# Kernel optimization log

Measured on AMD Instinct MI355X. Metric: run time of the kernel, lower is better.

## Reference

```python
import jax, jax.numpy as jnp
import numpy as np


def _conv(x, w, b, pad):
    y = jax.lax.conv_general_dilated(x, w, window_strides=(1, 1),
                                     padding=[(pad, pad), (pad, pad)],
                                     dimension_numbers=('NCHW', 'OIHW', 'NCHW'))
    return y + b[None, :, None, None]


def _kernel_normalizer(mask, k):
    # softmax over the k*k kernel taps; hamming=1 so the renorm is a numerical no-op (kept faithful)
    n, mck2, h, w = mask.shape
    mc = mck2 // (k * k)
    m = jax.nn.softmax(mask.reshape(n, mc, k * k, h, w), axis=2)
    m = m / jnp.sum(m, axis=2, keepdims=True)
    return m.reshape(n, mck2, h, w)


def _carafe(feat, mask, k, g, s):
    # CARAFE: out[n,c,i,j] = sum_{ki,kj} mask[n, grp*k*k + ki*k + kj, i, j] * feat[n, c, i//s+ki-r, j//s+kj-r]
    n, c, h, w = feat.shape
    r = (k - 1) // 2
    cg = c // g
    hs, ws = h * s, w * s
    pad = jnp.pad(feat, ((0, 0), (0, 0), (r, r), (r, r)))
    m = mask.reshape(n, g, k * k, hs, ws)
    out = jnp.zeros((n, g, cg, hs, ws), feat.dtype)
    idx = 0
    for ki in range(k):
        for kj in range(k):
            sh = pad[:, :, ki:ki + h, kj:kj + w]
            if s > 1:
                sh = jnp.repeat(jnp.repeat(sh, s, axis=2), s, axis=3)
            out = out + sh.reshape(n, g, cg, hs, ws) * m[:, :, idx][:, :, None]
            idx += 1
    return out.reshape(n, c, hs, ws)


def setup_inputs() -> dict:
    key = jax.random.key(0)
    ks = jax.random.split(key, 8)
    N, CH, CL, H, W, CC = 4, 256, 256, 128, 128, 64
    KL, KH, EK = 5, 3, 3

    def w_init(k, shape):
        fan_in = shape[1] * shape[2] * shape[3]
        return jax.random.normal(k, shape, jnp.float32) * (1.0 / np.sqrt(fan_in))

    return {
        'hr_feat': jax.random.normal(ks[0], (N, CH, H, W), jnp.float32),
        'lr_feat': jax.random.normal(ks[1], (N, CL, H // 2, W // 2), jnp.float32),
        'hr_w': w_init(ks[2], (CC, CH, 1, 1)), 'hr_b': jnp.zeros((CC,), jnp.float32),
        'lr_w': w_init(ks[3], (CC, CL, 1, 1)), 'lr_b': jnp.zeros((CC,), jnp.float32),
        'enc_w': w_init(ks[4], (KL * KL, CC, EK, EK)), 'enc_b': jnp.zeros((KL * KL,), jnp.float32),
        'enc2_w': w_init(ks[5], (KH * KH, CC, EK, EK)), 'enc2_b': jnp.zeros((KH * KH,), jnp.float32),
    }


def reference(hr_feat, lr_feat, hr_w, hr_b, lr_w, lr_b, enc_w, enc_b, enc2_w, enc2_b):
    KL, KH, G = 5, 3, 1
    chf = _conv(hr_feat, hr_w, hr_b, 0)
    clf = _conv(lr_feat, lr_w, lr_b, 0)
    mask_hr_hr = _conv(chf, enc2_w, enc2_b, 1)
    mask_hr_init = _kernel_normalizer(mask_hr_hr, KH)
    chf = chf + chf - _carafe(chf, mask_hr_init, KH, G, 1)
    mask_lr_hr = _conv(chf, enc_w, enc_b, 1)
    mask_lr_init = _kernel_normalizer(mask_lr_hr, KL)
    mask_lr_lr_lr = _conv(clf, enc_w, enc_b, 1)
    # carafe scale-2 output is already hr-sized -> F.interpolate(nearest, hr size) is identity
    mask_lr_lr = _carafe(mask_lr_lr_lr, mask_lr_init, KL, G, 2)
    mask_lr = mask_lr_hr + mask_lr_lr
    mask_lr_init = _kernel_normalizer(mask_lr, KL)
    mask_hr_lr = _carafe(_conv(clf, enc2_w, enc2_b, 1), mask_lr_init, KL, G, 2)
    mask_hr = mask_hr_hr + mask_hr_lr
    mask_lr_out = _kernel_normalizer(mask_lr, KL)
    lr_out = _carafe(lr_feat, mask_lr_out, KL, G, 2)
    mask_hr_out = _kernel_normalizer(mask_hr, KH)
    hr_out = (hr_feat - _carafe(hr_feat, mask_hr_out, KH, G, 1)) + hr_feat
    return (mask_lr_out, hr_out, lr_out)
```

## Files before the change

### kernel.cpp

```cpp
#include <hip/hip_runtime.h>
#include <hip/hip_bf16.h>

typedef __hip_bfloat16 bf16;

constexpr int Nn  = 4;
constexpr int Ci  = 256;
constexpr int Cc  = 64;
constexpr int Hh  = 128;
constexpr int Ww  = 128;
constexpr int HWh = Hh * Ww;
constexpr int Hl  = 64;
constexpr int Wl  = 64;
constexpr int HWl = Hl * Wl;
constexpr int K2L = 25;
constexpr int K2H = 9;

constexpr size_t OFF_MASK = 0;
constexpr size_t OFF_HR   = (size_t)Nn * K2L * HWh;
constexpr size_t OFF_LR   = OFF_HR + (size_t)Nn * Ci * HWh;

constexpr size_t A_CHF    = 0;
constexpr size_t A_MLRHR  = 0;
constexpr size_t A_MLRLL  = 1700000;
constexpr size_t A_CLFE2  = 2200000;
constexpr size_t A_MHRRAW = 4100000;
constexpr size_t A_WHR    = 7800000;
constexpr size_t A_WLR    = 7820000;
constexpr size_t A_WENC   = 7840000;
constexpr size_t A_WENC2  = 7860000;
constexpr size_t A_BHR    = 7870000;
constexpr size_t A_BLR    = 7870100;
constexpr size_t A_BENC   = 7870200;
constexpr size_t A_BENC2  = 7870300;

constexpr size_t B_CLF    = 0;
constexpr size_t B_CHF2   = 1100000;
constexpr size_t B_MHRHR  = 5300000;
constexpr size_t B_MLR    = 0;

__device__ __forceinline__ float tofloat(float v) { return v; }
__device__ __forceinline__ float tofloat(bf16 v) { return __bfloat162float(v); }

template<typename T> __device__ __forceinline__ T fromfloat(float v);
template<> __device__ __forceinline__ float fromfloat<float>(float v) { return v; }
template<> __device__ __forceinline__ bf16  fromfloat<bf16>(float v)  { return __float2bfloat16(v); }

__device__ __forceinline__ float* scrp(void* d, int f32, size_t reg, size_t off) {
  float* b = f32 ? ((float*)d + reg) : (float*)((bf16*)d + reg);
  return b + off;
}

__global__ void detect_dtype(const void* feat, int* flag) {
  __shared__ int s;
  if (threadIdx.x == 0) s = 0;
  __syncthreads();
  unsigned short b = ((const unsigned short*)feat)[threadIdx.x];
  float v = __uint_as_float(((unsigned int)b) << 16);
  if (!(fabsf(v) < 1000.0f)) atomicOr(&s, 1);
  __syncthreads();
  if (threadIdx.x == 0) *flag = s;
}

template<typename T>
__device__ void prep_body(const T* hw, const T* hb, const T* lw, const T* lb,
                          const T* ew, const T* eb, const T* e2w, const T* e2b,
                          float* whr, float* wlr, float* wenc, float* wenc2,
                          float* bhr, float* blr, float* benc, float* benc2) {
  int tid = blockIdx.x * 256 + threadIdx.x, nt = gridDim.x * 256;
  for (int i = tid; i < Cc * Ci; i += nt) {
    int co = i / Ci, ci = i % Ci;
    whr[ci * Cc + co] = tofloat(hw[i]);
    wlr[ci * Cc + co] = tofloat(lw[i]);
  }
  for (int i = tid; i < K2L * Cc * 9; i += nt) {
    int ko = i / (Cc * 9), r = i % (Cc * 9), ci = r / 9, k = r % 9;
    wenc[(ci * K2L + ko) * 9 + k] = tofloat(ew[i]);
  }
  for (int i = tid; i < K2H * Cc * 9; i += nt) {
    int ko = i / (Cc * 9), r = i % (Cc * 9), ci = r / 9, k = r % 9;
    wenc2[(ci * K2H + ko) * 9 + k] = tofloat(e2w[i]);
  }
  if (tid < Cc)  { bhr[tid] = tofloat(hb[tid]); blr[tid] = tofloat(lb[tid]); }
  if (tid < K2L) benc[tid]  = tofloat(eb[tid]);
  if (tid < K2H) benc2[tid] = tofloat(e2b[tid]);
}

__global__ void prep_weights(const int* flag, void* dout,
                             const void* hw, const void* hb, const void* lw, const void* lb,
                             const void* ew, const void* eb, const void* e2w, const void* e2b) {
  int f32 = *flag;
  float* whr   = scrp(dout, f32, OFF_LR, A_WHR);
  float* wlr   = scrp(dout, f32, OFF_LR, A_WLR);
  float* wenc  = scrp(dout, f32, OFF_LR, A_WENC);
  float* wenc2 = scrp(dout, f32, OFF_LR, A_WENC2);
  float* bhr   = scrp(dout, f32, OFF_LR, A_BHR);
  float* blr   = scrp(dout, f32, OFF_LR, A_BLR);
  float* benc  = scrp(dout, f32, OFF_LR, A_BENC);
  float* benc2 = scrp(dout, f32, OFF_LR, A_BENC2);
  if (f32) prep_body<float>((const float*)hw, (const float*)hb, (const float*)lw, (const float*)lb,
                            (const float*)ew, (const float*)eb, (const float*)e2w, (const float*)e2b,
                            whr, wlr, wenc, wenc2, bhr, blr, benc, benc2);
  else     prep_body<bf16>((const bf16*)hw, (const bf16*)hb, (const bf16*)lw, (const bf16*)lb,
                           (const bf16*)ew, (const bf16*)eb, (const bf16*)e2w, (const bf16*)e2b,
                           whr, wlr, wenc, wenc2, bhr, blr, benc, benc2);
}

template<typename T, int CW>
__device__ void conv1x1_body(const T* __restrict__ in, const float* __restrict__ wt,
                             const float* __restrict__ bias, float* __restrict__ out, int P) {
  const int tid = threadIdx.x;
  const int n = blockIdx.z;
  const int pbase = blockIdx.x * 64 + (tid & 63);
  const int co0 = __builtin_amdgcn_readfirstlane(blockIdx.y * 4 * CW + ((tid >> 6) * CW));
  const T* inp = in + (size_t)n * Ci * P + pbase;

  float acc[CW];
  #pragma unroll
  for (int c = 0; c < CW; ++c) acc[c] = bias[co0 + c];

  #pragma unroll 4
  for (int ci = 0; ci < Ci; ++ci) {
    float v = tofloat(inp[(size_t)ci * P]);
    const float* wr = wt + ci * Cc + co0;
    #pragma unroll
    for (int c = 0; c < CW; ++c) acc[c] = fmaf(v, wr[c], acc[c]);
  }
  float* op = out + (size_t)n * Cc * P + pbase;
  #pragma unroll
  for (int c = 0; c < CW; ++c) op[(size_t)(co0 + c) * P] = acc[c];
}

template<int CW>
__global__ __launch_bounds__(256) void conv1x1_k(const int* flag, void* dout, const void* in,
                                                 size_t w_off, size_t b_off,
                                                 size_t o_reg, size_t o_off, int P) {
  int f32 = __builtin_amdgcn_readfirstlane(*flag);
  const float* wt   = scrp(dout, f32, OFF_LR, w_off);
  const float* bias = scrp(dout, f32, OFF_LR, b_off);
  float* out        = scrp(dout, f32, o_reg, o_off);
  if (f32) conv1x1_body<float, CW>((const float*)in, wt, bias, out, P);
  else     conv1x1_body<bf16, CW>((const bf16*)in, wt, bias, out, P);
}

template<int KO, int KOG>
__device__ __forceinline__ void conv3x3_body(const float* __restrict__ in,
                                             const float* __restrict__ wt,
                                             const float* __restrict__ bias,
                                             float* __restrict__ out,
                                             int hh, int ww, int n, int ko0, float* tile) {
  const int tid = threadIdx.x;
  const int tx = tid & 15, ty = tid >> 4;
  const int bx = blockIdx.x * 16, by = blockIdx.y * 16;

  float acc[KOG];
  #pragma unroll
  for (int ko = 0; ko < KOG; ++ko) acc[ko] = bias[ko0 + ko];

  for (int cc = 0; cc < Cc; cc += 16) {
    __syncthreads();
    for (int i = tid; i < 16 * 18 * 18; i += 256) {
      int ci = i / 324, r = i % 324, yy = r / 18, xx = r % 18;
      int gy = by + yy - 1, gx = bx + xx - 1;
      float v = 0.f;
      if (gy >= 0 && gy < hh && gx >= 0 && gx < ww)
        v = in[(((size_t)n * Cc + cc + ci) * hh + gy) * ww + gx];
      tile[i] = v;
    }
    __syncthreads();
    for (int ci = 0; ci < 16; ++ci) {
      float nb[9];
      #pragma unroll
      for (int dy = 0; dy < 3; ++dy)
        #pragma unroll
        for (int dx = 0; dx < 3; ++dx)
          nb[dy * 3 + dx] = tile[ci * 324 + (ty + dy) * 18 + tx + dx];
      const float* wr = wt + ((size_t)(cc + ci) * KO + ko0) * 9;
      #pragma unroll
      for (int ko = 0; ko < KOG; ++ko)
        #pragma unroll
        for (int k = 0; k < 9; ++k)
          acc[ko] = fmaf(wr[ko * 9 + k], nb[k], acc[ko]);
    }
  }
  const size_t ob = (((size_t)n * KO + ko0) * hh + by + ty) * ww + bx + tx;
  #pragma unroll
  for (int ko = 0; ko < KOG; ++ko) out[ob + (size_t)ko * hh * ww] = acc[ko];
}

template<int KO, int KOG>
__global__ __launch_bounds__(256) void conv3x3_k(const int* flag, void* dout,
                                                 size_t i_reg, size_t i_off,
                                                 size_t w_off, size_t b_off,
                                                 size_t o_reg, size_t o_off, int hh, int ww) {
  const int f32 = __builtin_amdgcn_readfirstlane(*flag);
  const float* in   = scrp(dout, f32, i_reg, i_off);
  const float* wt   = scrp(dout, f32, OFF_LR, w_off);
  const float* bias = scrp(dout, f32, OFF_LR, b_off);
  float* out        = scrp(dout, f32, o_reg, o_off);

  constexpr int NG = KO / KOG;
  __shared__ float tile[16 * 18 * 18];
  const int n = blockIdx.z / NG;
  const int ko0 = (blockIdx.z % NG) * KOG;
  conv3x3_body<KO, KOG>(in, wt, bias, out, hh, ww, n, ko0, tile);
}

__global__ __launch_bounds__(256) void conv3x3_dual_k(const int* flag, void* dout) {
  const int f32 = __builtin_amdgcn_readfirstlane(*flag);
  const float* in    = scrp(dout, f32, OFF_HR, B_CLF);
  const float* wenc  = scrp(dout, f32, OFF_LR, A_WENC);
  const float* benc  = scrp(dout, f32, OFF_LR, A_BENC);
  const float* wenc2 = scrp(dout, f32, OFF_LR, A_WENC2);
  const float* benc2 = scrp(dout, f32, OFF_LR, A_BENC2);
  float* out_ll  = scrp(dout, f32, OFF_LR, A_MLRLL);
  float* out_e2  = scrp(dout, f32, OFF_LR, A_CLFE2);

  __shared__ float tile[16 * 18 * 18];
  const int g = blockIdx.z % 8;
  const int n = blockIdx.z / 8;
  if (g < 5) conv3x3_body<K2L, 5>(in, wenc, benc, out_ll, Hl, Wl, n, g * 5, tile);
  else       conv3x3_body<K2H, 3>(in, wenc2, benc2, out_e2, Hl, Wl, n, (g - 5) * 3, tile);
}

template<int K2>
__global__ __launch_bounds__(256) void softmax_k(const int* flag, void* dout,
                                                 size_t i_reg, size_t i_off) {
  int f32 = __builtin_amdgcn_readfirstlane(*flag);
  const float* in = scrp(dout, f32, i_reg, i_off);
  const int p = blockIdx.x * blockDim.x + threadIdx.x;
  const int n = blockIdx.y;
  const float* ip = in + (size_t)n * K2 * HWh + p;
  float v[K2], m = -1e30f;
  #pragma unroll
  for (int k = 0; k < K2; ++k) { v[k] = ip[(size_t)k * HWh]; m = fmaxf(m, v[k]); }
  float s = 0.f;
  #pragma unroll
  for (int k = 0; k < K2; ++k) { v[k] = __expf(v[k] - m); s += v[k]; }
  const float inv = 1.0f / s;
  #pragma unroll
  for (int k = 0; k < K2; ++k) v[k] *= inv;

  const size_t g = (size_t)n * K2 * HWh + p;
  if (f32) {
    float* o = (float*)dout;
    #pragma unroll
    for (int k = 0; k < K2; ++k) o[g + (size_t)k * HWh] = v[k];
  } else {
    bf16* o = (bf16*)dout;
    #pragma unroll
    for (int k = 0; k < K2; ++k) o[g + (size_t)k * HWh] = fromfloat<bf16>(v[k]);
  }
}

template<typename FT, typename OT, int FINAL, int SM>
__device__ void carafe1_body(const FT* __restrict__ feat, const float* __restrict__ mask,
                             void* dout, size_t out_reg, float* outscr, int C, int CPB) {
  const int tid = threadIdx.x;
  const int tx = tid & 15, ty = tid >> 4;
  const int bx = blockIdx.x * 16, by = blockIdx.y * 16;
  const int numCG = C / CPB;
  const int n = blockIdx.z / numCG, cg = blockIdx.z % numCG;
  const int x = bx + tx, y = by + ty;

  float mv[9];
  #pragma unroll
  for (int k = 0; k < 9; ++k)
    mv[k] = mask[(((size_t)n * 9 + k) * Hh + y) * Ww + x];
  if (SM) {
    float m = -1e30f;
    #pragma unroll
    for (int k = 0; k < 9; ++k) m = fmaxf(m, mv[k]);
    float s = 0.f;
    #pragma unroll
    for (int k = 0; k < 9; ++k) { mv[k] = __expf(mv[k] - m); s += mv[k]; }
    const float inv = 1.0f / s;
    #pragma unroll
    for (int k = 0; k < 9; ++k) mv[k] *= inv;
  }

  const int c0 = cg * CPB;
  for (int c = c0; c < c0 + CPB; ++c) {
    const FT* fp = feat + ((size_t)n * C + c) * HWh;
    float s = 0.f, center = 0.f;
    #pragma unroll
    for (int dy = -1; dy <= 1; ++dy)
      #pragma unroll
      for (int dx = -1; dx <= 1; ++dx) {
        int yy = y + dy, xx = x + dx;
        float fv = 0.f;
        if (yy >= 0 && yy < Hh && xx >= 0 && xx < Ww) fv = tofloat(fp[yy * Ww + xx]);
        if (dy == 0 && dx == 0) center = fv;
        s = fmaf(fv, mv[(dy + 1) * 3 + (dx + 1)], s);
      }
    float r = 2.f * center - s;
    const size_t li = ((size_t)n * C + c) * HWh + y * Ww + x;
    if (FINAL) ((OT*)dout)[out_reg + li] = fromfloat<OT>(r);
    else       outscr[li] = r;
  }
}

__global__ __launch_bounds__(256) void carafe1_scr_k(const int* flag, void* dout,
    size_t f_reg, size_t f_off, size_t m_reg, size_t m_off, size_t o_reg, size_t o_off,
    int C, int CPB) {
  int f32 = __builtin_amdgcn_readfirstlane(*flag);
  carafe1_body<float, float, 0, 1>(scrp(dout, f32, f_reg, f_off), scrp(dout, f32, m_reg, m_off),
                                   dout, 0, scrp(dout, f32, o_reg, o_off), C, CPB);
}

__global__ __launch_bounds__(256) void carafe1_io_k(const int* flag, void* dout, const void* feat,
    size_t m_reg, size_t m_off, size_t out_reg, int C, int CPB) {
  int f32 = __builtin_amdgcn_readfirstlane(*flag);
  const float* m = scrp(dout, f32, m_reg, m_off);
  if (f32) carafe1_body<float, float, 1, 1>((const float*)feat, m, dout, out_reg, nullptr, C, CPB);
  else     carafe1_body<bf16, bf16, 1, 1>((const bf16*)feat, m, dout, out_reg, nullptr, C, CPB);
}

template<typename FT, typename MT, typename OT, int ADD, int FINAL, int SM>
__device__ void carafe2_body(const FT* __restrict__ feat, const MT* __restrict__ mask,
                             const float* __restrict__ addend, void* dout, size_t out_reg,
                             float* outscr, int C, int CPB) {
  __shared__ float ft[8][144];
  const int tid = threadIdx.x;
  const int tx = tid & 15, ty = tid >> 4;
  const int bx = blockIdx.x * 16, by = blockIdx.y * 16;
  const int numCG = C / CPB;
  const int n = blockIdx.z / numCG, cg = blockIdx.z % numCG;
  const int x = bx + tx, y = by + ty;

  float mv[25];
  #pragma unroll
  for (int k = 0; k < 25; ++k)
    mv[k] = tofloat(mask[(((size_t)n * 25 + k) * Hh + y) * Ww + x]);
  if (SM) {
    float m = -1e30f;
    #pragma unroll
    for (int k = 0; k < 25; ++k) m = fmaxf(m, mv[k]);
    float s = 0.f;
    #pragma unroll
    for (int k = 0; k < 25; ++k) { mv[k] = __expf(mv[k] - m); s += mv[k]; }
    const float inv = 1.0f / s;
    #pragma unroll
    for (int k = 0; k < 25; ++k) mv[k] *= inv;
  }

  const int fy0 = (by >> 1) - 2, fx0 = (bx >> 1) - 2;
  const int fyb = (ty >> 1) + 2, fxb = (tx >> 1) + 2;
  const int c0 = cg * CPB;

  for (int cb = 0; cb < CPB; cb += 8) {
    const int lim = (CPB - cb < 8) ? (CPB - cb) : 8;
    __syncthreads();
    for (int i = tid; i < lim * 144; i += 256) {
      int cc = i / 144, r = i % 144, fy = r / 12, fx = r % 12;
      int gy = fy0 + fy, gx = fx0 + fx;
      float v = 0.f;
      if (gy >= 0 && gy < Hl && gx >= 0 && gx < Wl)
        v = tofloat(feat[((size_t)n * C + c0 + cb + cc) * HWl + gy * Wl + gx]);
      ft[cc][r] = v;
    }
    __syncthreads();
    for (int cc = 0; cc < lim; ++cc) {
      float s = 0.f;
      #pragma unroll
      for (int ki = 0; ki < 5; ++ki)
        #pragma unroll
        for (int kj = 0; kj < 5; ++kj)
          s = fmaf(ft[cc][(fyb + ki - 2) * 12 + (fxb + kj - 2)], mv[ki * 5 + kj], s);
      const size_t li = (((size_t)n * C + c0 + cb + cc) * Hh + y) * Ww + x;
      float r = ADD ? (addend[li] + s) : s;
      if (FINAL) ((OT*)dout)[out_reg + li] = fromfloat<OT>(r);
      else       outscr[li] = r;
    }
  }
}

__global__ __launch_bounds__(256) void carafe2_scr_k(const int* flag, void* dout,
    size_t f_reg, size_t f_off, size_t m_reg, size_t m_off, size_t a_reg, size_t a_off,
    size_t o_reg, size_t o_off, int C, int CPB) {
  int f32 = __builtin_amdgcn_readfirstlane(*flag);
  carafe2_body<float, float, float, 1, 0, 1>(scrp(dout, f32, f_reg, f_off), scrp(dout, f32, m_reg, m_off),
      scrp(dout, f32, a_reg, a_off), dout, 0, scrp(dout, f32, o_reg, o_off), C, CPB);
}

__global__ __launch_bounds__(256) void carafe2_m0_k(const int* flag, void* dout,
    size_t f_reg, size_t f_off, size_t a_reg, size_t a_off, size_t o_reg, size_t o_off,
    int C, int CPB) {
  int f32 = __builtin_amdgcn_readfirstlane(*flag);
  const float* f = scrp(dout, f32, f_reg, f_off);
  const float* a = scrp(dout, f32, a_reg, a_off);
  float* o = scrp(dout, f32, o_reg, o_off);
  if (f32) carafe2_body<float, float, float, 1, 0, 0>(f, (const float*)dout, a, dout, 0, o, C, CPB);
  else     carafe2_body<float, bf16, float, 1, 0, 0>(f, (const bf16*)dout, a, dout, 0, o, C, CPB);
}

__global__ __launch_bounds__(256) void carafe2_io_k(const int* flag, void* dout, const void* feat,
    size_t out_reg, int C, int CPB) {
  int f32 = __builtin_amdgcn_readfirstlane(*flag);
  if (f32) carafe2_body<float, float, float, 0, 1, 0>((const float*)feat, (const float*)dout,
      nullptr, dout, out_reg, nullptr, C, CPB);
  else     carafe2_body<bf16, bf16, bf16, 0, 1, 0>((const bf16*)feat, (const bf16*)dout,
      nullptr, dout, out_reg, nullptr, C, CPB);
}

extern "C" void kernel_launch(void* const* d_in, const int* in_sizes, int n_in,
                              void* d_out, int out_size, void* d_ws, size_t ws_size,
                              hipStream_t stream) {
  const void* hr_feat = d_in[0];
  const void* lr_feat = d_in[1];
  int* flag = (int*)d_ws;

  detect_dtype<<<1, 256, 0, stream>>>(hr_feat, flag);
  prep_weights<<<64, 256, 0, stream>>>(flag, d_out, d_in[2], d_in[3], d_in[4], d_in[5],
                                       d_in[6], d_in[7], d_in[8], d_in[9]);
  conv1x1_k<16><<<dim3(HWh / 64, 1, Nn), 256, 0, stream>>>(flag, d_out, hr_feat, A_WHR, A_BHR, OFF_LR, A_CHF, HWh);
  conv1x1_k<8><<<dim3(HWl / 64, 2, Nn), 256, 0, stream>>>(flag, d_out, lr_feat, A_WLR, A_BLR, OFF_HR, B_CLF, HWl);
  conv3x3_k<K2H, 3><<<dim3(8, 8, Nn * 3), 256, 0, stream>>>(flag, d_out, OFF_LR, A_CHF, A_WENC2, A_BENC2, OFF_HR, B_MHRHR, Hh, Ww);
  carafe1_scr_k<<<dim3(8, 8, Nn * (Cc / 16)), 256, 0, stream>>>(flag, d_out, OFF_LR, A_CHF, OFF_HR, B_MHRHR, OFF_HR, B_CHF2, Cc, 16);
  conv3x3_k<K2L, 5><<<dim3(8, 8, Nn * 5), 256, 0, stream>>>(flag, d_out, OFF_HR, B_CHF2, A_WENC, A_BENC, OFF_LR, A_MLRHR, Hh, Ww);
  conv3x3_dual_k<<<dim3(4, 4, Nn * 8), 256, 0, stream>>>(flag, d_out);
  carafe2_scr_k<<<dim3(8, 8, Nn * 5), 256, 0, stream>>>(flag, d_out, OFF_LR, A_MLRLL, OFF_LR, A_MLRHR,
                                                        OFF_LR, A_MLRHR, OFF_HR, B_MLR, K2L, 5);
  softmax_k<K2L><<<dim3(HWh / 128, Nn), 128, 0, stream>>>(flag, d_out, OFF_HR, B_MLR);
  carafe2_m0_k<<<dim3(8, 8, Nn * 3), 256, 0, stream>>>(flag, d_out, OFF_LR, A_CLFE2,
                                                       OFF_HR, B_MHRHR, OFF_LR, A_MHRRAW, K2H, 3);
  carafe1_io_k<<<dim3(8, 8, Nn * (Ci / 32)), 256, 0, stream>>>(flag, d_out, hr_feat,
                                                               OFF_LR, A_MHRRAW, OFF_HR, Ci, 32);
  carafe2_io_k<<<dim3(8, 8, Nn * (Ci / 32)), 256, 0, stream>>>(flag, d_out, lr_feat, OFF_LR, Ci, 32);
}
```

Before: 575.7 us.

## Fuse conv launches, fold softmax into carafe2, add interior fast paths

Merges the two 1x1 convolutions into one launch and merges the hr 3x3 encoder conv with the dual lr 3x3 conv into one launch using flattened block indices. The standalone softmax kernel is removed: carafe2_m0 now reads the raw mask_lr, normalises it in-kernel and writes the final mask_lr_out from its first channel group. Interior tiles skip the bounds checks in the conv3x3, carafe1 and carafe2 loads. Scratch offsets are moved so the fused kernels do not overwrite each other's buffers. This cuts launch count and one full pass over the mask, at the cost of more code paths and a redundant softmax per channel group.

```diff
diff --git a/kernel.cpp b/kernel.cpp
--- a/kernel.cpp
+++ b/kernel.cpp
@@ -21,9 +21,9 @@
 
 constexpr size_t A_CHF    = 0;
 constexpr size_t A_MLRHR  = 0;
-constexpr size_t A_MLRLL  = 1700000;
-constexpr size_t A_CLFE2  = 2200000;
-constexpr size_t A_MHRRAW = 4100000;
+constexpr size_t A_MLRLL  = 4300000;
+constexpr size_t A_CLFE2  = 4800000;
+constexpr size_t A_MHRRAW = 5000000;
 constexpr size_t A_WHR    = 7800000;
 constexpr size_t A_WLR    = 7820000;
 constexpr size_t A_WENC   = 7840000;
@@ -106,14 +106,10 @@
 }
 
 template<typename T, int CW>
-__device__ void conv1x1_body(const T* __restrict__ in, const float* __restrict__ wt,
-                             const float* __restrict__ bias, float* __restrict__ out, int P) {
-  const int tid = threadIdx.x;
-  const int n = blockIdx.z;
-  const int pbase = blockIdx.x * 64 + (tid & 63);
-  const int co0 = __builtin_amdgcn_readfirstlane(blockIdx.y * 4 * CW + ((tid >> 6) * CW));
+__device__ __forceinline__ void conv1x1_core(const T* __restrict__ in, const float* __restrict__ wt,
+                                             const float* __restrict__ bias, float* __restrict__ out,
+                                             int P, int n, int pbase, int co0) {
   const T* inp = in + (size_t)n * Ci * P + pbase;
-
   float acc[CW];
   #pragma unroll
   for (int c = 0; c < CW; ++c) acc[c] = bias[co0 + c];
@@ -130,16 +126,31 @@
   for (int c = 0; c < CW; ++c) op[(size_t)(co0 + c) * P] = acc[c];
 }
 
-template<int CW>
-__global__ __launch_bounds__(256) void conv1x1_k(const int* flag, void* dout, const void* in,
-                                                 size_t w_off, size_t b_off,
-                                                 size_t o_reg, size_t o_off, int P) {
-  int f32 = __builtin_amdgcn_readfirstlane(*flag);
-  const float* wt   = scrp(dout, f32, OFF_LR, w_off);
-  const float* bias = scrp(dout, f32, OFF_LR, b_off);
-  float* out        = scrp(dout, f32, o_reg, o_off);
-  if (f32) conv1x1_body<float, CW>((const float*)in, wt, bias, out, P);
-  else     conv1x1_body<bf16, CW>((const bf16*)in, wt, bias, out, P);
+__global__ __launch_bounds__(256) void conv1x1_both_k(const int* flag, void* dout,
+                                                      const void* hr, const void* lr) {
+  const int f32 = __builtin_amdgcn_readfirstlane(*flag);
+  const float* whr = scrp(dout, f32, OFF_LR, A_WHR);
+  const float* wlr = scrp(dout, f32, OFF_LR, A_WLR);
+  const float* bhr = scrp(dout, f32, OFF_LR, A_BHR);
+  const float* blr = scrp(dout, f32, OFF_LR, A_BLR);
+  float* ochf = scrp(dout, f32, OFF_LR, A_CHF);
+  float* oclf = scrp(dout, f32, OFF_HR, B_CLF);
+  const int tid = threadIdx.x;
+  int b = blockIdx.x;
+  if (b < Nn * 256) {
+    const int n = b >> 8, xb = b & 255;
+    const int pbase = xb * 64 + (tid & 63);
+    const int co0 = __builtin_amdgcn_readfirstlane((tid >> 6) * 16);
+    if (f32) conv1x1_core<float, 16>((const float*)hr, whr, bhr, ochf, HWh, n, pbase, co0);
+    else     conv1x1_core<bf16, 16>((const bf16*)hr, whr, bhr, ochf, HWh, n, pbase, co0);
+  } else {
+    b -= Nn * 256;
+    const int n = b >> 7, rem = b & 127;
+    const int pbase = (rem & 63) * 64 + (tid & 63);
+    const int co0 = __builtin_amdgcn_readfirstlane((rem >> 6) * 32 + (tid >> 6) * 8);
+    if (f32) conv1x1_core<float, 8>((const float*)lr, wlr, blr, oclf, HWl, n, pbase, co0);
+    else     conv1x1_core<bf16, 8>((const bf16*)lr, wlr, blr, oclf, HWl, n, pbase, co0);
+  }
 }
 
 template<int KO, int KOG>
@@ -147,10 +158,11 @@
                                              const float* __restrict__ wt,
                                              const float* __restrict__ bias,
                                              float* __restrict__ out,
-                                             int hh, int ww, int n, int ko0, float* tile) {
+                                             int hh, int ww, int n, int ko0,
+                                             int bx, int by, float* tile) {
   const int tid = threadIdx.x;
   const int tx = tid & 15, ty = tid >> 4;
-  const int bx = blockIdx.x * 16, by = blockIdx.y * 16;
+  const bool inter = (bx >= 16) && (by >= 16) && (bx + 32 <= ww) && (by + 32 <= hh);
 
   float acc[KOG];
   #pragma unroll
@@ -158,13 +170,20 @@
 
   for (int cc = 0; cc < Cc; cc += 16) {
     __syncthreads();
-    for (int i = tid; i < 16 * 18 * 18; i += 256) {
-      int ci = i / 324, r = i % 324, yy = r / 18, xx = r % 18;
-      int gy = by + yy - 1, gx = bx + xx - 1;
-      float v = 0.f;
-      if (gy >= 0 && gy < hh && gx >= 0 && gx < ww)
-        v = in[(((size_t)n * Cc + cc + ci) * hh + gy) * ww + gx];
-      tile[i] = v;
+    if (inter) {
+      for (int i = tid; i < 16 * 324; i += 256) {
+        int ci = i / 324, r = i % 324, yy = r / 18, xx = r % 18;
+        tile[i] = in[(((size_t)n * Cc + cc + ci) * hh + by + yy - 1) * ww + bx + xx - 1];
+      }
+    } else {
+      for (int i = tid; i < 16 * 324; i += 256) {
+        int ci = i / 324, r = i % 324, yy = r / 18, xx = r % 18;
+        int gy = by + yy - 1, gx = bx + xx - 1;
+        float v = 0.f;
+        if (gy >= 0 && gy < hh && gx >= 0 && gx < ww)
+          v = in[(((size_t)n * Cc + cc + ci) * hh + gy) * ww + gx];
+        tile[i] = v;
+      }
     }
     __syncthreads();
     for (int ci = 0; ci < 16; ++ci) {
@@ -199,56 +218,36 @@
   float* out        = scrp(dout, f32, o_reg, o_off);
 
   constexpr int NG = KO / KOG;
-  __shared__ float tile[16 * 18 * 18];
+  __shared__ float tile[16 * 324];
   const int n = blockIdx.z / NG;
   const int ko0 = (blockIdx.z % NG) * KOG;
-  conv3x3_body<KO, KOG>(in, wt, bias, out, hh, ww, n, ko0, tile);
-}
-
-__global__ __launch_bounds__(256) void conv3x3_dual_k(const int* flag, void* dout) {
+  conv3x3_body<KO, KOG>(in, wt, bias, out, hh, ww, n, ko0, blockIdx.x * 16, blockIdx.y * 16, tile);
+}
+
+__global__ __launch_bounds__(256) void fused_s3_k(const int* flag, void* dout) {
   const int f32 = __builtin_amdgcn_readfirstlane(*flag);
-  const float* in    = scrp(dout, f32, OFF_HR, B_CLF);
+  const float* chf   = scrp(dout, f32, OFF_LR, A_CHF);
+  const float* clf   = scrp(dout, f32, OFF_HR, B_CLF);
   const float* wenc  = scrp(dout, f32, OFF_LR, A_WENC);
   const float* benc  = scrp(dout, f32, OFF_LR, A_BENC);
   const float* wenc2 = scrp(dout, f32, OFF_LR, A_WENC2);
   const float* benc2 = scrp(dout, f32, OFF_LR, A_BENC2);
-  float* out_ll  = scrp(dout, f32, OFF_LR, A_MLRLL);
-  float* out_e2  = scrp(dout, f32, OFF_LR, A_CLFE2);
-
-  __shared__ float tile[16 * 18 * 18];
-  const int g = blockIdx.z % 8;
-  const int n = blockIdx.z / 8;
-  if (g < 5) conv3x3_body<K2L, 5>(in, wenc, benc, out_ll, Hl, Wl, n, g * 5, tile);
-  else       conv3x3_body<K2H, 3>(in, wenc2, benc2, out_e2, Hl, Wl, n, (g - 5) * 3, tile);
-}
-
-template<int K2>
-__global__ __launch_bounds__(256) void softmax_k(const int* flag, void* dout,
-                                                 size_t i_reg, size_t i_off) {
-  int f32 = __builtin_amdgcn_readfirstlane(*flag);
-  const float* in = scrp(dout, f32, i_reg, i_off);
-  const int p = blockIdx.x * blockDim.x + threadIdx.x;
-  const int n = blockIdx.y;
-  const float* ip = in + (size_t)n * K2 * HWh + p;
-  float v[K2], m = -1e30f;
-  #pragma unroll
-  for (int k = 0; k < K2; ++k) { v[k] = ip[(size_t)k * HWh]; m = fmaxf(m, v[k]); }
-  float s = 0.f;
-  #pragma unroll
-  for (int k = 0; k < K2; ++k) { v[k] = __expf(v[k] - m); s += v[k]; }
-  const float inv = 1.0f / s;
-  #pragma unroll
-  for (int k = 0; k < K2; ++k) v[k] *= inv;
-
-  const size_t g = (size_t)n * K2 * HWh + p;
-  if (f32) {
-    float* o = (float*)dout;
-    #pragma unroll
-    for (int k = 0; k < K2; ++k) o[g + (size_t)k * HWh] = v[k];
+  float* o_mhrhr = scrp(dout, f32, OFF_HR, B_MHRHR);
+  float* o_ll    = scrp(dout, f32, OFF_LR, A_MLRLL);
+  float* o_e2    = scrp(dout, f32, OFF_LR, A_CLFE2);
+  __shared__ float tile[16 * 324];
+  int b = blockIdx.x;
+  if (b < Nn * 3 * 64) {
+    const int z = b >> 6, rem = b & 63;
+    conv3x3_body<K2H, 3>(chf, wenc2, benc2, o_mhrhr, Hh, Ww, z / 3, (z % 3) * 3,
+                         (rem & 7) * 16, (rem >> 3) * 16, tile);
   } else {
-    bf16* o = (bf16*)dout;
-    #pragma unroll
-    for (int k = 0; k < K2; ++k) o[g + (size_t)k * HWh] = fromfloat<bf16>(v[k]);
+    b -= Nn * 3 * 64;
+    const int z = b >> 4, rem = b & 15;
+    const int bx = (rem & 3) * 16, by = (rem >> 2) * 16;
+    const int g = z & 7, n = z >> 3;
+    if (g < 5) conv3x3_body<K2L, 5>(clf, wenc, benc, o_ll, Hl, Wl, n, g * 5, bx, by, tile);
+    else       conv3x3_body<K2H, 3>(clf, wenc2, benc2, o_e2, Hl, Wl, n, (g - 5) * 3, bx, by, tile);
   }
 }
 
@@ -261,6 +260,7 @@
   const int numCG = C / CPB;
   const int n = blockIdx.z / numCG, cg = blockIdx.z % numCG;
   const int x = bx + tx, y = by + ty;
+  const bool inter = (bx >= 16) && (by >= 16) && (bx + 32 <= Ww) && (by + 32 <= Hh);
 
   float mv[9];
   #pragma unroll
@@ -279,23 +279,40 @@
   }
 
   const int c0 = cg * CPB;
-  for (int c = c0; c < c0 + CPB; ++c) {
-    const FT* fp = feat + ((size_t)n * C + c) * HWh;
-    float s = 0.f, center = 0.f;
-    #pragma unroll
-    for (int dy = -1; dy <= 1; ++dy)
+  if (inter) {
+    for (int c = c0; c < c0 + CPB; ++c) {
+      const FT* fp = feat + ((size_t)n * C + c) * HWh + (size_t)y * Ww + x;
+      float center = tofloat(fp[0]);
+      float s = 0.f;
       #pragma unroll
-      for (int dx = -1; dx <= 1; ++dx) {
-        int yy = y + dy, xx = x + dx;
-        float fv = 0.f;
-        if (yy >= 0 && yy < Hh && xx >= 0 && xx < Ww) fv = tofloat(fp[yy * Ww + xx]);
-        if (dy == 0 && dx == 0) center = fv;
-        s = fmaf(fv, mv[(dy + 1) * 3 + (dx + 1)], s);
-      }
-    float r = 2.f * center - s;
-    const size_t li = ((size_t)n * C + c) * HWh + y * Ww + x;
-    if (FINAL) ((OT*)dout)[out_reg + li] = fromfloat<OT>(r);
-    else       outscr[li] = r;
+      for (int dy = -1; dy <= 1; ++dy)
+        #pragma unroll
+        for (int dx = -1; dx <= 1; ++dx)
+          s = fmaf(tofloat(fp[dy * Ww + dx]), mv[(dy + 1) * 3 + (dx + 1)], s);
+      float r = 2.f * center - s;
+      const size_t li = ((size_t)n * C + c) * HWh + (size_t)y * Ww + x;
+      if (FINAL) ((OT*)dout)[out_reg + li] = fromfloat<OT>(r);
+      else       outscr[li] = r;
+    }
+  } else {
+    for (int c = c0; c < c0 + CPB; ++c) {
+      const FT* fp = feat + ((size_t)n * C + c) * HWh;
+      float s = 0.f, center = 0.f;
+      #pragma unroll
+      for (int dy = -1; dy <= 1; ++dy)
+        #pragma unroll
+        for (int dx = -1; dx <= 1; ++dx) {
+          int yy = y + dy, xx = x + dx;
+          float fv = 0.f;
+          if (yy >= 0 && yy < Hh && xx >= 0 && xx < Ww) fv = tofloat(fp[yy * Ww + xx]);
+          if (dy == 0 && dx == 0) center = fv;
+          s = fmaf(fv, mv[(dy + 1) * 3 + (dx + 1)], s);
+        }
+      float r = 2.f * center - s;
+      const size_t li = ((size_t)n * C + c) * HWh + (size_t)y * Ww + x;
+      if (FINAL) ((OT*)dout)[out_reg + li] = fromfloat<OT>(r);
+      else       outscr[li] = r;
+    }
   }
 }
 
@@ -315,7 +332,7 @@
   else     carafe1_body<bf16, bf16, 1, 1>((const bf16*)feat, m, dout, out_reg, nullptr, C, CPB);
 }
 
-template<typename FT, typename MT, typename OT, int ADD, int FINAL, int SM>
+template<typename FT, typename MT, typename OT, typename MOT, int ADD, int FINAL, int SM, int WMASK>
 __device__ void carafe2_body(const FT* __restrict__ feat, const MT* __restrict__ mask,
                              const float* __restrict__ addend, void* dout, size_t out_reg,
                              float* outscr, int C, int CPB) {
@@ -326,6 +343,7 @@
   const int numCG = C / CPB;
   const int n = blockIdx.z / numCG, cg = blockIdx.z % numCG;
   const int x = bx + tx, y = by + ty;
+  const bool inter = (bx >= 16) && (by >= 16) && (bx + 32 <= Ww) && (by + 32 <= Hh);
 
   float mv[25];
   #pragma unroll
@@ -342,6 +360,12 @@
     #pragma unroll
     for (int k = 0; k < 25; ++k) mv[k] *= inv;
   }
+  if (WMASK && cg == 0) {
+    const size_t g = (size_t)n * 25 * HWh + (size_t)y * Ww + x;
+    MOT* mo = (MOT*)dout;
+    #pragma unroll
+    for (int k = 0; k < 25; ++k) mo[g + (size_t)k * HWh] = fromfloat<MOT>(mv[k]);
+  }
 
   const int fy0 = (by >> 1) - 2, fx0 = (bx >> 1) - 2;
   const int fyb = (ty >> 1) + 2, fxb = (tx >> 1) + 2;
@@ -350,13 +374,20 @@
   for (int cb = 0; cb < CPB; cb += 8) {
     const int lim = (CPB - cb < 8) ? (CPB - cb) : 8;
     __syncthreads();
-    for (int i = tid; i < lim * 144; i += 256) {
-      int cc = i / 144, r = i % 144, fy = r / 12, fx = r % 12;
-      int gy = fy0 + fy, gx = fx0 + fx;
-      float v = 0.f;
-      if (gy >= 0 && gy < Hl && gx >= 0 && gx < Wl)
-        v = tofloat(feat[((size_t)n * C + c0 + cb + cc) * HWl + gy * Wl + gx]);
-      ft[cc][r] = v;
+    if (inter) {
+      for (int i = tid; i < lim * 144; i += 256) {
+        int cc = i / 144, r = i % 144, fy = r / 12, fx = r % 12;
+        ft[cc][r] = tofloat(feat[((size_t)n * C + c0 + cb + cc) * HWl + (fy0 + fy) * Wl + fx0 + fx]);
+      }
+    } else {
+      for (int i = tid; i < lim * 144; i += 256) {
+        int cc = i / 144, r = i % 144, fy = r / 12, fx = r % 12;
+        int gy = fy0 + fy, gx = fx0 + fx;
+        float v = 0.f;
+        if (gy >= 0 && gy < Hl && gx >= 0 && gx < Wl)
+          v = tofloat(feat[((size_t)n * C + c0 + cb + cc) * HWl + gy * Wl + gx]);
+        ft[cc][r] = v;
+      }
     }
     __syncthreads();
     for (int cc = 0; cc < lim; ++cc) {
@@ -378,27 +409,29 @@
     size_t f_reg, size_t f_off, size_t m_reg, size_t m_off, size_t a_reg, size_t a_off,
     size_t o_reg, size_t o_off, int C, int CPB) {
   int f32 = __builtin_amdgcn_readfirstlane(*flag);
-  carafe2_body<float, float, float, 1, 0, 1>(scrp(dout, f32, f_reg, f_off), scrp(dout, f32, m_reg, m_off),
+  carafe2_body<float, float, float, float, 1, 0, 1, 0>(
+      scrp(dout, f32, f_reg, f_off), scrp(dout, f32, m_reg, m_off),
       scrp(dout, f32, a_reg, a_off), dout, 0, scrp(dout, f32, o_reg, o_off), C, CPB);
 }
 
 __global__ __launch_bounds__(256) void carafe2_m0_k(const int* flag, void* dout,
-    size_t f_reg, size_t f_off, size_t a_reg, size_t a_off, size_t o_reg, size_t o_off,
-    int C, int CPB) {
+    size_t f_reg, size_t f_off, size_t m_reg, size_t m_off, size_t a_reg, size_t a_off,
+    size_t o_reg, size_t o_off, int C, int CPB) {
   int f32 = __builtin_amdgcn_readfirstlane(*flag);
   const float* f = scrp(dout, f32, f_reg, f_off);
+  const float* m = scrp(dout, f32, m_reg, m_off);
   const float* a = scrp(dout, f32, a_reg, a_off);
   float* o = scrp(dout, f32, o_reg, o_off);
-  if (f32) carafe2_body<float, float, float, 1, 0, 0>(f, (const float*)dout, a, dout, 0, o, C, CPB);
-  else     carafe2_body<float, bf16, float, 1, 0, 0>(f, (const bf16*)dout, a, dout, 0, o, C, CPB);
+  if (f32) carafe2_body<float, float, float, float, 1, 0, 1, 1>(f, m, a, dout, 0, o, C, CPB);
+  else     carafe2_body<float, float, float, bf16, 1, 0, 1, 1>(f, m, a, dout, 0, o, C, CPB);
 }
 
 __global__ __launch_bounds__(256) void carafe2_io_k(const int* flag, void* dout, const void* feat,
     size_t out_reg, int C, int CPB) {
   int f32 = __builtin_amdgcn_readfirstlane(*flag);
-  if (f32) carafe2_body<float, float, float, 0, 1, 0>((const float*)feat, (const float*)dout,
+  if (f32) carafe2_body<float, float, float, float, 0, 1, 0, 0>((const float*)feat, (const float*)dout,
       nullptr, dout, out_reg, nullptr, C, CPB);
-  else     carafe2_body<bf16, bf16, bf16, 0, 1, 0>((const bf16*)feat, (const bf16*)dout,
+  else     carafe2_body<bf16, bf16, bf16, bf16, 0, 1, 0, 0>((const bf16*)feat, (const bf16*)dout,
       nullptr, dout, out_reg, nullptr, C, CPB);
 }
 
@@ -412,17 +445,15 @@
   detect_dtype<<<1, 256, 0, stream>>>(hr_feat, flag);
   prep_weights<<<64, 256, 0, stream>>>(flag, d_out, d_in[2], d_in[3], d_in[4], d_in[5],
                                        d_in[6], d_in[7], d_in[8], d_in[9]);
-  conv1x1_k<16><<<dim3(HWh / 64, 1, Nn), 256, 0, stream>>>(flag, d_out, hr_feat, A_WHR, A_BHR, OFF_LR, A_CHF, HWh);
-  conv1x1_k<8><<<dim3(HWl / 64, 2, Nn), 256, 0, stream>>>(flag, d_out, lr_feat, A_WLR, A_BLR, OFF_HR, B_CLF, HWl);
-  conv3x3_k<K2H, 3><<<dim3(8, 8, Nn * 3), 256, 0, stream>>>(flag, d_out, OFF_LR, A_CHF, A_WENC2, A_BENC2, OFF_HR, B_MHRHR, Hh, Ww);
+  conv1x1_both_k<<<Nn * 256 + Nn * 128, 256, 0, stream>>>(flag, d_out, hr_feat, lr_feat);
+  fused_s3_k<<<Nn * 3 * 64 + Nn * 8 * 16, 256, 0, stream>>>(flag, d_out);
   carafe1_scr_k<<<dim3(8, 8, Nn * (Cc / 16)), 256, 0, stream>>>(flag, d_out, OFF_LR, A_CHF, OFF_HR, B_MHRHR, OFF_HR, B_CHF2, Cc, 16);
   conv3x3_k<K2L, 5><<<dim3(8, 8, Nn * 5), 256, 0, stream>>>(flag, d_out, OFF_HR, B_CHF2, A_WENC, A_BENC, OFF_LR, A_MLRHR, Hh, Ww);
-  conv3x3_dual_k<<<dim3(4, 4, Nn * 8), 256, 0, stream>>>(flag, d_out);
   carafe2_scr_k<<<dim3(8, 8, Nn * 5), 256, 0, stream>>>(flag, d_out, OFF_LR, A_MLRLL, OFF_LR, A_MLRHR,
                                                         OFF_LR, A_MLRHR, OFF_HR, B_MLR, K2L, 5);
-  softmax_k<K2L><<<dim3(HWh / 128, Nn), 128, 0, stream>>>(flag, d_out, OFF_HR, B_MLR);
   carafe2_m0_k<<<dim3(8, 8, Nn * 3), 256, 0, stream>>>(flag, d_out, OFF_LR, A_CLFE2,
-                                                       OFF_HR, B_MHRHR, OFF_LR, A_MHRRAW, K2H, 3);
+                                                       OFF_HR, B_MLR, OFF_HR, B_MHRHR,
+                                                       OFF_LR, A_MHRRAW, K2H, 3);
   carafe1_io_k<<<dim3(8, 8, Nn * (Ci / 32)), 256, 0, stream>>>(flag, d_out, hr_feat,
                                                                OFF_LR, A_MHRRAW, OFF_HR, Ci, 32);
   carafe2_io_k<<<dim3(8, 8, Nn * (Ci / 32)), 256, 0, stream>>>(flag, d_out, lr_feat, OFF_LR, Ci, 32);
```

Result: slower. 677.8 us (+17.7%).
